# Performance work log

Hardware: AMD Instinct MI355X
Metric: run time of the kernel (lower is better)

## Reference

```python
import jax, jax.numpy as jnp
import numpy as np

L = 18                      # tree depth, N = 2**L - 1 nodes (complete binary tree)
N = 2**L - 1               # 262143
D = 128                     # embedding dim
V = 100000                  # vocab size of the single data type
E = 8                       # edge_count


def setup_inputs() -> dict:
    key = jax.random.key(0)
    ks = jax.random.split(key, 8)
    data = jax.random.randint(ks[0], (N,), 0, V)
    edges = jax.random.randint(ks[1], (N,), 0, E)
    data_vecs = jax.random.normal(ks[2], (V, D), dtype=jnp.float32) * 0.1
    # torch uses torch.rand (U[0,1)); scaled for numerical stability over 18 levels
    data_W = jax.random.uniform(ks[3], (D, D), dtype=jnp.float32) * 0.1
    data_b = jax.random.uniform(ks[4], (D,), dtype=jnp.float32) * 0.1
    edge_W = jax.random.uniform(ks[5], (E, D, D), dtype=jnp.float32) * (2.0 / D)
    edge_b = jax.random.uniform(ks[6], (E, D), dtype=jnp.float32) * 0.1
    score_W = jax.random.uniform(ks[7], (D, 1), dtype=jnp.float32)
    return {"data": data, "edges": edges, "data_vecs": data_vecs,
            "data_W": data_W, "data_b": data_b, "edge_W": edge_W,
            "edge_b": edge_b, "score_W": score_W}


def reference(data, edges, data_vecs, data_W, data_b, edge_W, edge_b, score_W):
    # per-node leaf term: addmm(data_bias, data_vecs[data], data_W)  -> [N, D]
    raw = data_vecs[data] @ data_W + data_b
    ret = raw    # value returned to the parent (leaves: unclamped)
    emb = raw    # stored embedding (internal nodes: pre-clamp h)
    # bottom-up over levels; level l occupies indices [2**l - 1, 2**(l+1) - 1)
    for l in reversed(range(L - 1)):
        p0, npar = 2**l - 1, 2**l
        c0, M = 2**(l + 1) - 1, 2**(l + 1)
        child_ret = ret[c0:c0 + M]              # [M, D], siblings adjacent
        eids = edges[c0:c0 + M]                 # [M]
        # edge-weighted child transform: child @ edge_W[e] + edge_b[e]
        contrib = edge_b[eids]
        for e in range(E):                      # small static edge loop
            contrib = contrib + jnp.where((eids == e)[:, None], child_ret, 0.0) @ edge_W[e]
        # sum the two children of each parent, then (leaf + children) / (nc + 1)
        contrib = contrib.reshape(npar, 2, D).sum(axis=1)
        h = (raw[p0:p0 + npar] + contrib) / 3.0
        emb = emb.at[p0:p0 + npar].set(h)
        ret = ret.at[p0:p0 + npar].set(jnp.maximum(h, 0.0))
    scores = (emb @ score_W)[:, 0]              # [N]
    return scores


if __name__ == "__main__":
    out = reference(**setup_inputs())
    print(out.shape, out.dtype)
```

## Files before the change

kernel.cpp:

```cpp
#include <hip/hip_runtime.h>

#define D 128
#define NLVL 17
#define TS 64
#define LVLPAD 1024
#define LDSTR 136
#define LEAF_BLKS 2057
#define CHUNK 2048
#define CNT_BLKS 128
#define PLVL0 10
#define CBASE 2047
#define NBINS 56
#define NRAW 2047

typedef float  floatx4 __attribute__((ext_vector_type(4)));
typedef short  shortx8 __attribute__((ext_vector_type(8)));

__device__ __forceinline__ unsigned short f2bf(float f) {
    unsigned u = __float_as_uint(f);
    u += 0x7FFFu + ((u >> 16) & 1u);
    return (unsigned short)(u >> 16);
}
__device__ __forceinline__ float bf2f(unsigned short h) {
    return __uint_as_float(((unsigned)h) << 16);
}
__device__ __forceinline__ int lvl_base_dev(int l) { return ((2 << l) - 2) + LVLPAD * l; }

__global__ __launch_bounds__(256) void prep_kernel(
    const float* __restrict__ dW, const float* __restrict__ db,
    const float* __restrict__ eW, const float* __restrict__ eb,
    const float* __restrict__ sWs, const float* __restrict__ vecs,
    const int* __restrict__ edges,
    unsigned short* __restrict__ ewt, unsigned short* __restrict__ cwt,
    unsigned short* __restrict__ dwt, float* __restrict__ dcomp,
    float* __restrict__ sv, float* __restrict__ s0, int* __restrict__ ctr,
    int* __restrict__ gcnt128, int Nn,
    unsigned short* __restrict__ vbf, int n4)
{
    __shared__ float smem[8448];
    const int b = blockIdx.x, t = threadIdx.x;
    if (b < 32) {
        float* w_s = smem;
        float* cs  = smem + 4096;
        const int e = b >> 2, cc = b & 3;
        for (int i = t; i < D * 8; i += 256) {
            const int k = i >> 3, j4 = i & 7;
            ((float4*)w_s)[i] = ((const float4*)eW)[((size_t)e * D + k) * 32 + cc * 8 + j4];
        }
        __syncthreads();
        const int r2 = t >> 1, h = t & 1;
        float4 acc[4];
        #pragma unroll
        for (int m = 0; m < 4; m++) acc[m] = make_float4(0.f, 0.f, 0.f, 0.f);
        for (int k = 0; k < D; k++) {
            const float a = dW[(size_t)r2 * D + k];
            #pragma unroll
            for (int m = 0; m < 4; m++) {
                const float4 w4 = ((const float4*)w_s)[k * 8 + h * 4 + m];
                acc[m].x += a * w4.x; acc[m].y += a * w4.y; acc[m].z += a * w4.z; acc[m].w += a * w4.w;
            }
        }
        #pragma unroll
        for (int m = 0; m < 4; m++) {
            cs[r2 * 33 + h * 16 + m * 4 + 0] = acc[m].x;
            cs[r2 * 33 + h * 16 + m * 4 + 1] = acc[m].y;
            cs[r2 * 33 + h * 16 + m * 4 + 2] = acc[m].z;
            cs[r2 * 33 + h * 16 + m * 4 + 3] = acc[m].w;
        }
        __syncthreads();
        {
            const int nn = t >> 3, kseg = t & 7, k0 = kseg * 16;
            unsigned ow[8];
            #pragma unroll
            for (int i2 = 0; i2 < 8; i2++) {
                const unsigned short lo = f2bf(cs[(k0 + 2 * i2) * 33 + nn]);
                const unsigned short hi = f2bf(cs[(k0 + 2 * i2 + 1) * 33 + nn]);
                ow[i2] = (unsigned)lo | ((unsigned)hi << 16);
            }
            uint4* dstp = (uint4*)(cwt + (size_t)e * D * D + (size_t)(cc * 32 + nn) * D + k0);
            dstp[0] = make_uint4(ow[0], ow[1], ow[2], ow[3]);
            dstp[1] = make_uint4(ow[4], ow[5], ow[6], ow[7]);
        }
        if (t < 32) {
            float a2 = 0.f;
            for (int k = 0; k < D; k++) a2 += db[k] * w_s[k * 32 + t];
            dcomp[e * D + cc * 32 + t] = a2 + eb[e * D + cc * 32 + t];
        }
    } else if (b < 41) {
        float* lds = smem;
        const int bb = b - 32;
        const float* src = (bb < 8) ? (eW + (size_t)bb * D * D) : dW;
        unsigned short* dst = (bb < 8) ? (ewt + (size_t)bb * D * D) : dwt;
        for (int half = 0; half < 2; half++) {
            __syncthreads();
            for (int i = t; i < 64 * D / 4; i += 256) {
                float4 v = ((const float4*)src)[half * (64 * D / 4) + i];
                const int k = (i * 4) >> 7, n = (i * 4) & 127;
                lds[k * 129 + n]     = v.x;
                lds[k * 129 + n + 1] = v.y;
                lds[k * 129 + n + 2] = v.z;
                lds[k * 129 + n + 3] = v.w;
            }
            __syncthreads();
            const int n = t >> 1, hh = t & 1;
            for (int kk = 0; kk < 32; kk++) {
                const int k = hh * 32 + kk;
                dst[(size_t)n * D + half * 64 + k] = f2bf(lds[k * 129 + n]);
            }
        }
    } else if (b == 41) {
        float* red = smem;
        if (t < NBINS) ctr[t] = 0;
        if (t < D) {
            float acc = 0.f;
            for (int j = 0; j < D; j++) acc += dW[(size_t)t * D + j] * sWs[j];
            sv[t] = acc;
        }
        red[t] = (t < D) ? db[t] * sWs[t] : 0.f;
        __syncthreads();
        for (int s = 128; s > 0; s >>= 1) { if (t < s) red[t] += red[t + s]; __syncthreads(); }
        if (t == 0) s0[0] = red[0];
    } else if (b < 42 + CNT_BLKS) {
        int* lc = (int*)smem;
        if (t < NBINS) lc[t] = 0;
        __syncthreads();
        for (int c = CBASE + (b - 42) * 256 + t; c < Nn; c += CNT_BLKS * 256) {
            const int e = edges[c];
            const int p = (c - 1) >> 1;
            const int l = 31 - __clz(p + 1);
            atomicAdd(&lc[(l - PLVL0) * 8 + e], 1);
        }
        __syncthreads();
        if (t < NBINS) gcnt128[(b - 42) * NBINS + t] = lc[t];
    } else {
        for (int i = (b - 42 - CNT_BLKS) * 256 + t; i < n4; i += (gridDim.x - 42 - CNT_BLKS) * 256) {
            const float4 v = ((const float4*)vecs)[i];
            uint2 o;
            o.x = (unsigned)f2bf(v.x) | ((unsigned)f2bf(v.y) << 16);
            o.y = (unsigned)f2bf(v.z) | ((unsigned)f2bf(v.w) << 16);
            ((uint2*)vbf)[i] = o;
        }
    }
}

__global__ __launch_bounds__(256) void place_kernel(
    const int* __restrict__ edges, const int* __restrict__ gcnt128,
    int* __restrict__ gstart, int* __restrict__ glim,
    int* __restrict__ ctr, int* __restrict__ perm, int Nn)
{
    __shared__ unsigned char key_s[CHUNK];
    __shared__ int part[256];
    __shared__ int tot[NBINS];
    __shared__ int lcnt[NBINS], lbase[NBINS];
    __shared__ int gs_s[7 * 9], gl_s[7 * 8];
    const int t = threadIdx.x;
    {
        const int k = t & 63, bs = t >> 6;
        int s = 0;
        if (k < NBINS)
            for (int bb = bs; bb < CNT_BLKS; bb += 4) s += gcnt128[bb * NBINS + k];
        part[t] = s;
    }
    if (t < NBINS) lcnt[t] = 0;
    __syncthreads();
    if (t < NBINS)
        tot[t] = part[t] + part[t + 64] + part[t + 128] + part[t + 192];
    __syncthreads();
    if (t == 0) {
        for (int li = 0; li < 7; li++) {
            int acc = 0;
            for (int e = 0; e < 8; e++) {
                gs_s[li * 9 + e] = acc;
                gl_s[li * 8 + e] = acc + tot[li * 8 + e];
                acc = (acc + tot[li * 8 + e] + (TS - 1)) & ~(TS - 1);
            }
            gs_s[li * 9 + 8] = acc;
        }
    }
    __syncthreads();
    if (blockIdx.x == 0) {
        if (t < 63) gstart[PLVL0 * 9 + t] = gs_s[t];
        if (t < NBINS) glim[PLVL0 * 8 + t] = gl_s[t];
    }
    const int base = CBASE + blockIdx.x * CHUNK;
    for (int i = t; i < CHUNK; i += 256) {
        const int c = base + i;
        if (c < Nn) {
            const int e = edges[c];
            const int p = (c - 1) >> 1;
            const int l = 31 - __clz(p + 1);
            const int kk = (l - PLVL0) * 8 + e;
            key_s[i] = (unsigned char)kk;
            atomicAdd(&lcnt[kk], 1);
        } else key_s[i] = 255;
    }
    __syncthreads();
    if (t < NBINS) {
        const int n = lcnt[t];
        lbase[t] = n ? atomicAdd(&ctr[t], n) : 0;
        lcnt[t] = 0;
    }
    __syncthreads();
    for (int i = t; i < CHUNK; i += 256) {
        const int c = base + i;
        if (c >= Nn) continue;
        const int kk = key_s[i];
        if (kk == 255) continue;
        const int off = atomicAdd(&lcnt[kk], 1);
        const int l = (kk >> 3) + PLVL0, e = kk & 7;
        const int pos = gs_s[(l - PLVL0) * 9 + e] + lbase[kk] + off;
        perm[lvl_base_dev(l) + pos] = c;
    }
}

__global__ __launch_bounds__(256, 6) void leaf_embed_kernel(
    unsigned short* __restrict__ X,
    const unsigned short* __restrict__ vbf,
    const int* __restrict__ data,
    const int* __restrict__ perm,
    const int* __restrict__ gstart9,
    const int* __restrict__ glim8,
    const unsigned short* __restrict__ cwt,
    const float* __restrict__ dcomp,
    const float* __restrict__ sv, const float* __restrict__ s0p,
    const unsigned short* __restrict__ dwt,
    const float* __restrict__ db,
    float* __restrict__ out,
    int NI, int lbase_leaf)
{
    __shared__ unsigned short a_s[TS * LDSTR];
    const int t = threadIdx.x;
    const bool is_leaf = (blockIdx.x < LEAF_BLKS);
    const int r = t >> 2, h4 = t & 3;

    int e = 0, c;
    const unsigned short* Wg;
    const float* bias;
    if (is_leaf) {
        const int ts = blockIdx.x * TS;
        if (ts >= gstart9[8]) return;
        #pragma unroll
        for (int j = 1; j < 8; j++) if (ts >= gstart9[j]) e = j;
        const int p = ts + r;
        c = (p < glim8[e]) ? perm[lbase_leaf + p] : -1;
        Wg = cwt + (size_t)e * D * D;
        bias = dcomp + (size_t)e * D;
    } else {
        const int node = (blockIdx.x - LEAF_BLKS) * TS + r;
        c = (node < NI) ? node : -1;
        Wg = dwt;
        bias = db;
    }

    {
        unsigned short* dst = a_s + r * LDSTR + h4 * 32;
        if (c >= 0) {
            const uint4* src = (const uint4*)(vbf + (size_t)data[c] * D + h4 * 32);
            if (is_leaf) {
                float sc = 0.f;
                #pragma unroll
                for (int j = 0; j < 4; j++) {
                    const uint4 v = src[j];
                    const unsigned* pv = (const unsigned*)&v;
                    #pragma unroll
                    for (int u = 0; u < 4; u++) {
                        const int n = h4 * 32 + j * 8 + u * 2;
                        sc += bf2f((unsigned short)pv[u]) * sv[n]
                            + bf2f((unsigned short)(pv[u] >> 16)) * sv[n + 1];
                    }
                    ((uint4*)dst)[j] = v;
                }
                sc += __shfl_xor(sc, 1, 64);
                sc += __shfl_xor(sc, 2, 64);
                if (h4 == 0) out[c] = sc + s0p[0];
            } else {
                #pragma unroll
                for (int j = 0; j < 4; j++) ((uint4*)dst)[j] = src[j];
            }
        } else {
            #pragma unroll
            for (int j = 0; j < 4; j++) ((uint4*)dst)[j] = make_uint4(0u, 0u, 0u, 0u);
        }
    }
    __syncthreads();

    const int lane = t & 63, wv = t >> 6;
    const int cq = lane & 15, q = lane >> 4;
    const floatx4 z4 = {0.f, 0.f, 0.f, 0.f};
    floatx4 acc[4][2];
    #pragma unroll
    for (int i = 0; i < 4; i++) { acc[i][0] = z4; acc[i][1] = z4; }
    #pragma unroll
    for (int ks = 0; ks < 4; ks++) {
        shortx8 bfr[2];
        #pragma unroll
        for (int nl = 0; nl < 2; nl++) {
            const int n = (wv * 2 + nl) * 16 + cq;
            bfr[nl] = *(const shortx8*)(Wg + (size_t)n * D + ks * 32 + q * 8);
        }
        #pragma unroll
        for (int mt = 0; mt < 4; mt++) {
            const shortx8 af = *(const shortx8*)(a_s + (mt * 16 + cq) * LDSTR + ks * 32 + q * 8);
            acc[mt][0] = __builtin_amdgcn_mfma_f32_16x16x32_bf16(bfr[0], af, acc[mt][0], 0, 0, 0);
            acc[mt][1] = __builtin_amdgcn_mfma_f32_16x16x32_bf16(bfr[1], af, acc[mt][1], 0, 0, 0);
        }
    }
    __syncthreads();
    #pragma unroll
    for (int nl = 0; nl < 2; nl++) {
        const int n0 = (wv * 2 + nl) * 16 + q * 4;
        const float4 b4 = *(const float4*)(bias + n0);
        #pragma unroll
        for (int mt = 0; mt < 4; mt++) {
            const int m = mt * 16 + cq;
            const unsigned lo = (unsigned)f2bf(acc[mt][nl][0] + b4.x)
                              | ((unsigned)f2bf(acc[mt][nl][1] + b4.y) << 16);
            const unsigned hi = (unsigned)f2bf(acc[mt][nl][2] + b4.z)
                              | ((unsigned)f2bf(acc[mt][nl][3] + b4.w) << 16);
            *(uint2*)(a_s + (size_t)m * LDSTR + n0) = make_uint2(lo, hi);
        }
    }
    __syncthreads();
    if (c >= 0) {
        uint4* dstg = (uint4*)(X + (size_t)c * D + h4 * 32);
        const uint4* srcl = (const uint4*)(a_s + r * LDSTR + h4 * 32);
        #pragma unroll
        for (int j = 0; j < 4; j++) dstg[j] = srcl[j];
    }
}

__global__ __launch_bounds__(256, 3) void tree_fused_kernel(
    unsigned short* __restrict__ X,
    const unsigned short* __restrict__ vbf,
    const int* __restrict__ data,
    const int* __restrict__ perm,
    const int* __restrict__ gstart9,
    const int* __restrict__ glim8,
    const unsigned short* __restrict__ dwt,
    const float* __restrict__ db,
    const unsigned short* __restrict__ ewt,
    const float* __restrict__ eb,
    const float* __restrict__ svec,
    float* __restrict__ out,
    int lbase)
{
    __shared__ unsigned short a_s[TS * LDSTR];
    __shared__ float cs_s[TS][132];
    __shared__ float scorebuf[TS];
    const int t = threadIdx.x;
    const int ts = blockIdx.x * TS;
    if (ts >= gstart9[8]) return;
    int e = 0;
    #pragma unroll
    for (int j = 1; j < 8; j++) if (ts >= gstart9[j]) e = j;
    const int r = t >> 2, h4 = t & 3;
    const int p = ts + r;
    const int c = (p < glim8[e]) ? perm[lbase + p] : -1;

    if (t < TS) scorebuf[t] = 0.f;
    {
        unsigned short* dst = a_s + r * LDSTR + h4 * 32;
        float* cd = &cs_s[r][h4 * 32];
        if (c >= 0) {
            const uint4* src = (const uint4*)(vbf + (size_t)data[c] * D + h4 * 32);
            const uint4* ya = (const uint4*)(X + (size_t)(2 * c + 1) * D + h4 * 32);
            const uint4* yb = (const uint4*)(X + (size_t)(2 * c + 2) * D + h4 * 32);
            #pragma unroll
            for (int j = 0; j < 4; j++) {
                ((uint4*)dst)[j] = src[j];
                const uint4 rb = ya[j], rc = yb[j];
                const unsigned* pb = (const unsigned*)&rb;
                const unsigned* pc = (const unsigned*)&rc;
                #pragma unroll
                for (int u = 0; u < 4; u++) {
                    cd[j * 8 + u * 2]     = bf2f((unsigned short)pb[u]) + bf2f((unsigned short)pc[u]);
                    cd[j * 8 + u * 2 + 1] = bf2f((unsigned short)(pb[u] >> 16)) + bf2f((unsigned short)(pc[u] >> 16));
                }
            }
        } else {
            #pragma unroll
            for (int j = 0; j < 4; j++) {
                ((uint4*)dst)[j] = make_uint4(0u, 0u, 0u, 0u);
                ((float4*)cd)[j * 2]     = make_float4(0.f, 0.f, 0.f, 0.f);
                ((float4*)cd)[j * 2 + 1] = make_float4(0.f, 0.f, 0.f, 0.f);
            }
        }
    }
    __syncthreads();

    const int lane = t & 63, wv = t >> 6;
    const int cq = lane & 15, q = lane >> 4;
    const floatx4 z4 = {0.f, 0.f, 0.f, 0.f};
    floatx4 acc[4][2];
    #pragma unroll
    for (int i = 0; i < 4; i++) { acc[i][0] = z4; acc[i][1] = z4; }
    #pragma unroll
    for (int ks = 0; ks < 4; ks++) {
        shortx8 bfr[2];
        #pragma unroll
        for (int nl = 0; nl < 2; nl++) {
            const int n = (wv * 2 + nl) * 16 + cq;
            bfr[nl] = *(const shortx8*)(dwt + (size_t)n * D + ks * 32 + q * 8);
        }
        #pragma unroll
        for (int mt = 0; mt < 4; mt++) {
            const shortx8 af = *(const shortx8*)(a_s + (mt * 16 + cq) * LDSTR + ks * 32 + q * 8);
            acc[mt][0] = __builtin_amdgcn_mfma_f32_16x16x32_bf16(bfr[0], af, acc[mt][0], 0, 0, 0);
            acc[mt][1] = __builtin_amdgcn_mfma_f32_16x16x32_bf16(bfr[1], af, acc[mt][1], 0, 0, 0);
        }
    }
    const float inv3 = 1.0f / 3.0f;
    float sp[4] = {0.f, 0.f, 0.f, 0.f};
    uint2 hpk[2][4];
    #pragma unroll
    for (int nl = 0; nl < 2; nl++) {
        const int n0 = (wv * 2 + nl) * 16 + q * 4;
        const float4 db4 = *(const float4*)(db + n0);
        const float4 sv4 = *(const float4*)(svec + n0);
        #pragma unroll
        for (int mt = 0; mt < 4; mt++) {
            const int m = mt * 16 + cq;
            const float4 cs4 = *(const float4*)(&cs_s[m][n0]);
            const float h0 = (acc[mt][nl][0] + db4.x + cs4.x) * inv3;
            const float h1 = (acc[mt][nl][1] + db4.y + cs4.y) * inv3;
            const float h2 = (acc[mt][nl][2] + db4.z + cs4.z) * inv3;
            const float h3 = (acc[mt][nl][3] + db4.w + cs4.w) * inv3;
            sp[mt] += h0 * sv4.x + h1 * sv4.y + h2 * sv4.z + h3 * sv4.w;
            unsigned short q0 = f2bf(h0), q1 = f2bf(h1), q2 = f2bf(h2), q3 = f2bf(h3);
            q0 = (q0 & 0x8000u) ? 0 : q0;
            q1 = (q1 & 0x8000u) ? 0 : q1;
            q2 = (q2 & 0x8000u) ? 0 : q2;
            q3 = (q3 & 0x8000u) ? 0 : q3;
            hpk[nl][mt] = make_uint2((unsigned)q0 | ((unsigned)q1 << 16),
                                     (unsigned)q2 | ((unsigned)q3 << 16));
        }
    }
    #pragma unroll
    for (int mt = 0; mt < 4; mt++) {
        sp[mt] += __shfl_xor(sp[mt], 16, 64);
        sp[mt] += __shfl_xor(sp[mt], 32, 64);
    }
    __syncthreads();
    #pragma unroll
    for (int nl = 0; nl < 2; nl++) {
        const int n0 = (wv * 2 + nl) * 16 + q * 4;
        #pragma unroll
        for (int mt = 0; mt < 4; mt++)
            *(uint2*)(a_s + (size_t)(mt * 16 + cq) * LDSTR + n0) = hpk[nl][mt];
    }
    if (q == 0) {
        #pragma unroll
        for (int mt = 0; mt < 4; mt++) atomicAdd(&scorebuf[mt * 16 + cq], sp[mt]);
    }
    __syncthreads();
    const unsigned short* Wg = ewt + (size_t)e * D * D;
    #pragma unroll
    for (int i = 0; i < 4; i++) { acc[i][0] = z4; acc[i][1] = z4; }
    #pragma unroll
    for (int ks = 0; ks < 4; ks++) {
        shortx8 bfr[2];
        #pragma unroll
        for (int nl = 0; nl < 2; nl++) {
            const int n = (wv * 2 + nl) * 16 + cq;
            bfr[nl] = *(const shortx8*)(Wg + (size_t)n * D + ks * 32 + q * 8);
        }
        #pragma unroll
        for (int mt = 0; mt < 4; mt++) {
            const shortx8 af = *(const shortx8*)(a_s + (mt * 16 + cq) * LDSTR + ks * 32 + q * 8);
            acc[mt][0] = __builtin_amdgcn_mfma_f32_16x16x32_bf16(bfr[0], af, acc[mt][0], 0, 0, 0);
            acc[mt][1] = __builtin_amdgcn_mfma_f32_16x16x32_bf16(bfr[1], af, acc[mt][1], 0, 0, 0);
        }
    }
    __syncthreads();
    #pragma unroll
    for (int nl = 0; nl < 2; nl++) {
        const int n0 = (wv * 2 + nl) * 16 + q * 4;
        const float4 b4 = *(const float4*)(eb + (size_t)e * D + n0);
        #pragma unroll
        for (int mt = 0; mt < 4; mt++) {
            const int m = mt * 16 + cq;
            const unsigned lo = (unsigned)f2bf(acc[mt][nl][0] + b4.x)
                              | ((unsigned)f2bf(acc[mt][nl][1] + b4.y) << 16);
            const unsigned hi = (unsigned)f2bf(acc[mt][nl][2] + b4.z)
                              | ((unsigned)f2bf(acc[mt][nl][3] + b4.w) << 16);
            *(uint2*)(a_s + (size_t)m * LDSTR + n0) = make_uint2(lo, hi);
        }
    }
    __syncthreads();
    if (c >= 0) {
        uint4* dstg = (uint4*)(X + (size_t)c * D + h4 * 32);
        const uint4* srcl = (const uint4*)(a_s + r * LDSTR + h4 * 32);
        #pragma unroll
        for (int j = 0; j < 4; j++) dstg[j] = srcl[j];
        if (h4 == 1) out[c] = scorebuf[r];
    }
}

__global__ __launch_bounds__(256) void sub_kernel(
    unsigned short* __restrict__ X,
    const float* __restrict__ eW,
    const float* __restrict__ eb,
    const int* __restrict__ edges,
    const float* __restrict__ sW,
    float* __restrict__ out,
    int rbase, int nlev)
{
    __shared__ __align__(16) float xbuf[4][D];
    const int t = threadIdx.x, wv = t >> 6, lane = t & 63;
    const int u = rbase + blockIdx.x;
    const int j2 = lane * 2;
    const float inv3 = 1.0f / 3.0f;

    for (int lev = nlev - 1; lev >= 0; lev--) {
        const int first = ((u + 1) << lev) - 1;
        const int cnt = 1 << lev;
        for (int i = wv; i < cnt; i += 4) {
            const int n = first + i;
            const unsigned ra = *(const unsigned*)(X + (size_t)n * D + j2);
            const unsigned rb = *(const unsigned*)(X + (size_t)(2 * n + 1) * D + j2);
            const unsigned rc = *(const unsigned*)(X + (size_t)(2 * n + 2) * D + j2);
            const float h0 = (bf2f((unsigned short)ra) + bf2f((unsigned short)rb)
                            + bf2f((unsigned short)rc)) * inv3;
            const float h1 = (bf2f((unsigned short)(ra >> 16)) + bf2f((unsigned short)(rb >> 16))
                            + bf2f((unsigned short)(rc >> 16))) * inv3;
            float sc = h0 * sW[j2] + h1 * sW[j2 + 1];
            #pragma unroll
            for (int o = 32; o > 0; o >>= 1) sc += __shfl_xor(sc, o, 64);
            if (lane == 0) out[n] = sc;
            if (n == 0) continue;
            float2 x2 = make_float2(fmaxf(h0, 0.f), fmaxf(h1, 0.f));
            *(float2*)(xbuf[wv] + j2) = x2;
            const int e = edges[n];
            const float* W = eW + (size_t)e * D * D;
            float y0 = 0.f, y1 = 0.f;
            #pragma unroll 8
            for (int k4 = 0; k4 < 32; k4++) {
                const float4 xk = *(const float4*)(xbuf[wv] + k4 * 4);
                const float2 w0 = *(const float2*)(W + (size_t)(k4 * 4 + 0) * D + j2);
                const float2 w1 = *(const float2*)(W + (size_t)(k4 * 4 + 1) * D + j2);
                const float2 w2 = *(const float2*)(W + (size_t)(k4 * 4 + 2) * D + j2);
                const float2 w3 = *(const float2*)(W + (size_t)(k4 * 4 + 3) * D + j2);
                y0 += xk.x * w0.x + xk.y * w1.x + xk.z * w2.x + xk.w * w3.x;
                y1 += xk.x * w0.y + xk.y * w1.y + xk.z * w2.y + xk.w * w3.y;
            }
            y0 += eb[e * D + j2];
            y1 += eb[e * D + j2 + 1];
            const unsigned o = (unsigned)f2bf(y0) | ((unsigned)f2bf(y1) << 16);
            *(unsigned*)(X + (size_t)n * D + j2) = o;
        }
        __syncthreads();
    }
}

extern "C" void kernel_launch(void* const* d_in, const int* in_sizes, int n_in,
                              void* d_out, int out_size, void* d_ws, size_t ws_size,
                              hipStream_t stream) {
    const int*   data      = (const int*)d_in[0];
    const int*   edges     = (const int*)d_in[1];
    const float* data_vecs = (const float*)d_in[2];
    const float* data_W    = (const float*)d_in[3];
    const float* data_b    = (const float*)d_in[4];
    const float* edge_W    = (const float*)d_in[5];
    const float* edge_b    = (const float*)d_in[6];
    const float* score_W   = (const float*)d_in[7];
    float* out = (float*)d_out;

    const int Nn = in_sizes[0];
    const int VD = in_sizes[2];
    const int PERM_TOTAL = (Nn - 1) + LVLPAD * NLVL;

    char* w = (char*)d_ws;
    size_t off = 0;
    unsigned short* X = (unsigned short*)(w + off); off += (size_t)Nn * D * 2;
    int* perm = (int*)(w + off);  off += (size_t)PERM_TOTAL * 4;
    off = (off + 255) & ~(size_t)255;
    int* gstart  = (int*)(w + off); off += NLVL * 9 * 4;
    int* glim    = (int*)(w + off); off += NLVL * 8 * 4;
    int* gcnt128 = (int*)(w + off); off += CNT_BLKS * 64 * 4;
    int* ctr     = (int*)(w + off); off += 64 * 4;
    off = (off + 255) & ~(size_t)255;
    float* dcomp = (float*)(w + off); off += 8 * D * 4;
    float* sv    = (float*)(w + off); off += D * 4;
    float* s0    = (float*)(w + off); off += 256;
    off = (off + 255) & ~(size_t)255;
    unsigned short* ewt = (unsigned short*)(w + off); off += (size_t)8 * D * D * 2;
    unsigned short* cwt = (unsigned short*)(w + off); off += (size_t)8 * D * D * 2;
    unsigned short* dwt = (unsigned short*)(w + off); off += (size_t)D * D * 2;
    off = (off + 255) & ~(size_t)255;
    unsigned short* vbf = (unsigned short*)(w + off); off += (size_t)VD * 2;

    prep_kernel<<<42 + CNT_BLKS + 1024, 256, 0, stream>>>(
        data_W, data_b, edge_W, edge_b, score_W, data_vecs, edges,
        ewt, cwt, dwt, dcomp, sv, s0, ctr, gcnt128, Nn, vbf, VD / 4);

    const int place_blks = (Nn - CBASE + CHUNK - 1) / CHUNK;
    place_kernel<<<place_blks, 256, 0, stream>>>(edges, gcnt128, gstart, glim, ctr, perm, Nn);

    {
        const int embed_blks = (NRAW + TS - 1) / TS;
        const int lbase_leaf = ((2 << 16) - 2) + LVLPAD * 16;
        leaf_embed_kernel<<<LEAF_BLKS + embed_blks, 256, 0, stream>>>(
            X, vbf, data, perm, gstart + 16 * 9, glim + 16 * 8,
            cwt, dcomp, sv, s0, dwt, data_b, out, NRAW, lbase_leaf);
    }

    for (int l = 15; l >= PLVL0; l--) {
        const int M = 2 << l;
        const int lbase = ((2 << l) - 2) + LVLPAD * l;
        tree_fused_kernel<<<M / TS + 8, 256, 0, stream>>>(
            X, vbf, data, perm, gstart + l * 9, glim + l * 8,
            dwt, data_b, ewt, edge_b, score_W, out, lbase);
    }

    sub_kernel<<<128, 256, 0, stream>>>(X, edge_W, edge_b, edges, score_W, out, 127, 4);
    sub_kernel<<<8, 256, 0, stream>>>(X, edge_W, edge_b, edges, score_W, out, 7, 4);
    sub_kernel<<<1, 256, 0, stream>>>(X, edge_W, edge_b, edges, score_W, out, 0, 3);
}
```

Baseline: 283.4 us.

## Merge all stages into one persistent cooperative kernel with grid syncs

Replaces the sequence of about eleven kernel launches (prep, place, leaf embed, six tree levels, three sub kernels) with one cooperative persistent kernel. Each former kernel becomes a device function run over virtual block indices in a grid-stride loop, with grid.sync() between stages and shared memory pooled in one static buffer. This removes per-launch overhead and the gaps between dependent launches. In exchange, the grid is capped at 768 blocks with occupancy limited by the largest shared-memory stage, grid-wide barriers add their own cost, and the serial sub stages leave most blocks idle.

```diff
diff --git a/kernel.cpp b/kernel.cpp
--- a/kernel.cpp
+++ b/kernel.cpp
@@ -1,4 +1,7 @@
 #include <hip/hip_runtime.h>
+#include <hip/hip_cooperative_groups.h>
+
+namespace cg = cooperative_groups;
 
 #define D 128
 #define NLVL 17
@@ -12,6 +15,8 @@
 #define CBASE 2047
 #define NBINS 56
 #define NRAW 2047
+#define VEC_BLKS 1024
+#define SPOOL_BYTES 51456
 
 typedef float  floatx4 __attribute__((ext_vector_type(4)));
 typedef short  shortx8 __attribute__((ext_vector_type(8)));
@@ -26,26 +31,45 @@
 }
 __device__ __forceinline__ int lvl_base_dev(int l) { return ((2 << l) - 2) + LVLPAD * l; }
 
-__global__ __launch_bounds__(256) void prep_kernel(
-    const float* __restrict__ dW, const float* __restrict__ db,
-    const float* __restrict__ eW, const float* __restrict__ eb,
-    const float* __restrict__ sWs, const float* __restrict__ vecs,
-    const int* __restrict__ edges,
-    unsigned short* __restrict__ ewt, unsigned short* __restrict__ cwt,
-    unsigned short* __restrict__ dwt, float* __restrict__ dcomp,
-    float* __restrict__ sv, float* __restrict__ s0, int* __restrict__ ctr,
-    int* __restrict__ gcnt128, int Nn,
-    unsigned short* __restrict__ vbf, int n4)
+struct MegaArgs {
+    const int*   data;
+    const int*   edges;
+    const float* vecs;
+    const float* dW;
+    const float* db;
+    const float* eW;
+    const float* eb;
+    const float* sWs;
+    unsigned short* X;
+    int* perm;
+    int* gstart;
+    int* glim;
+    int* gcnt;
+    int* ctr;
+    float* dcomp;
+    float* sv;
+    float* s0;
+    unsigned short* ewt;
+    unsigned short* cwt;
+    unsigned short* dwt;
+    unsigned short* vbf;
+    float* out;
+    int Nn;
+    int n4;
+};
+
+__device__ void prep_block(int b, const MegaArgs& A, char* spool)
 {
-    __shared__ float smem[8448];
-    const int b = blockIdx.x, t = threadIdx.x;
+    const int t = threadIdx.x;
+    float* smem = (float*)spool;
+    __syncthreads();
     if (b < 32) {
         float* w_s = smem;
         float* cs  = smem + 4096;
         const int e = b >> 2, cc = b & 3;
         for (int i = t; i < D * 8; i += 256) {
             const int k = i >> 3, j4 = i & 7;
-            ((float4*)w_s)[i] = ((const float4*)eW)[((size_t)e * D + k) * 32 + cc * 8 + j4];
+            ((float4*)w_s)[i] = ((const float4*)A.eW)[((size_t)e * D + k) * 32 + cc * 8 + j4];
         }
         __syncthreads();
         const int r2 = t >> 1, h = t & 1;
@@ -53,7 +77,7 @@
         #pragma unroll
         for (int m = 0; m < 4; m++) acc[m] = make_float4(0.f, 0.f, 0.f, 0.f);
         for (int k = 0; k < D; k++) {
-            const float a = dW[(size_t)r2 * D + k];
+            const float a = A.dW[(size_t)r2 * D + k];
             #pragma unroll
             for (int m = 0; m < 4; m++) {
                 const float4 w4 = ((const float4*)w_s)[k * 8 + h * 4 + m];
@@ -77,20 +101,20 @@
                 const unsigned short hi = f2bf(cs[(k0 + 2 * i2 + 1) * 33 + nn]);
                 ow[i2] = (unsigned)lo | ((unsigned)hi << 16);
             }
-            uint4* dstp = (uint4*)(cwt + (size_t)e * D * D + (size_t)(cc * 32 + nn) * D + k0);
+            uint4* dstp = (uint4*)(A.cwt + (size_t)e * D * D + (size_t)(cc * 32 + nn) * D + k0);
             dstp[0] = make_uint4(ow[0], ow[1], ow[2], ow[3]);
             dstp[1] = make_uint4(ow[4], ow[5], ow[6], ow[7]);
         }
         if (t < 32) {
             float a2 = 0.f;
-            for (int k = 0; k < D; k++) a2 += db[k] * w_s[k * 32 + t];
-            dcomp[e * D + cc * 32 + t] = a2 + eb[e * D + cc * 32 + t];
+            for (int k = 0; k < D; k++) a2 += A.db[k] * w_s[k * 32 + t];
+            A.dcomp[e * D + cc * 32 + t] = a2 + A.eb[e * D + cc * 32 + t];
         }
     } else if (b < 41) {
         float* lds = smem;
         const int bb = b - 32;
-        const float* src = (bb < 8) ? (eW + (size_t)bb * D * D) : dW;
-        unsigned short* dst = (bb < 8) ? (ewt + (size_t)bb * D * D) : dwt;
+        const float* src = (bb < 8) ? (A.eW + (size_t)bb * D * D) : A.dW;
+        unsigned short* dst = (bb < 8) ? (A.ewt + (size_t)bb * D * D) : A.dwt;
         for (int half = 0; half < 2; half++) {
             __syncthreads();
             for (int i = t; i < 64 * D / 4; i += 256) {
@@ -110,55 +134,55 @@
         }
     } else if (b == 41) {
         float* red = smem;
-        if (t < NBINS) ctr[t] = 0;
+        if (t < NBINS) A.ctr[t] = 0;
         if (t < D) {
             float acc = 0.f;
-            for (int j = 0; j < D; j++) acc += dW[(size_t)t * D + j] * sWs[j];
-            sv[t] = acc;
-        }
-        red[t] = (t < D) ? db[t] * sWs[t] : 0.f;
+            for (int j = 0; j < D; j++) acc += A.dW[(size_t)t * D + j] * A.sWs[j];
+            A.sv[t] = acc;
+        }
+        red[t] = (t < D) ? A.db[t] * A.sWs[t] : 0.f;
         __syncthreads();
         for (int s = 128; s > 0; s >>= 1) { if (t < s) red[t] += red[t + s]; __syncthreads(); }
-        if (t == 0) s0[0] = red[0];
+        if (t == 0) A.s0[0] = red[0];
     } else if (b < 42 + CNT_BLKS) {
         int* lc = (int*)smem;
         if (t < NBINS) lc[t] = 0;
         __syncthreads();
-        for (int c = CBASE + (b - 42) * 256 + t; c < Nn; c += CNT_BLKS * 256) {
-            const int e = edges[c];
+        for (int c = CBASE + (b - 42) * 256 + t; c < A.Nn; c += CNT_BLKS * 256) {
+            const int e = A.edges[c];
             const int p = (c - 1) >> 1;
             const int l = 31 - __clz(p + 1);
             atomicAdd(&lc[(l - PLVL0) * 8 + e], 1);
         }
         __syncthreads();
-        if (t < NBINS) gcnt128[(b - 42) * NBINS + t] = lc[t];
+        if (t < NBINS) A.gcnt[(b - 42) * NBINS + t] = lc[t];
     } else {
-        for (int i = (b - 42 - CNT_BLKS) * 256 + t; i < n4; i += (gridDim.x - 42 - CNT_BLKS) * 256) {
-            const float4 v = ((const float4*)vecs)[i];
+        for (int i = (b - 42 - CNT_BLKS) * 256 + t; i < A.n4; i += VEC_BLKS * 256) {
+            const float4 v = ((const float4*)A.vecs)[i];
             uint2 o;
             o.x = (unsigned)f2bf(v.x) | ((unsigned)f2bf(v.y) << 16);
             o.y = (unsigned)f2bf(v.z) | ((unsigned)f2bf(v.w) << 16);
-            ((uint2*)vbf)[i] = o;
-        }
-    }
-}
-
-__global__ __launch_bounds__(256) void place_kernel(
-    const int* __restrict__ edges, const int* __restrict__ gcnt128,
-    int* __restrict__ gstart, int* __restrict__ glim,
-    int* __restrict__ ctr, int* __restrict__ perm, int Nn)
+            ((uint2*)A.vbf)[i] = o;
+        }
+    }
+}
+
+__device__ void place_block(int vb, const MegaArgs& A, char* spool)
 {
-    __shared__ unsigned char key_s[CHUNK];
-    __shared__ int part[256];
-    __shared__ int tot[NBINS];
-    __shared__ int lcnt[NBINS], lbase[NBINS];
-    __shared__ int gs_s[7 * 9], gl_s[7 * 8];
+    unsigned char* key_s = (unsigned char*)spool;
+    int* part  = (int*)(spool + 2048);
+    int* tot   = (int*)(spool + 3072);
+    int* lcnt  = (int*)(spool + 3328);
+    int* lbase = (int*)(spool + 3584);
+    int* gs_s  = (int*)(spool + 3840);
+    int* gl_s  = (int*)(spool + 4096);
     const int t = threadIdx.x;
+    __syncthreads();
     {
         const int k = t & 63, bs = t >> 6;
         int s = 0;
         if (k < NBINS)
-            for (int bb = bs; bb < CNT_BLKS; bb += 4) s += gcnt128[bb * NBINS + k];
+            for (int bb = bs; bb < CNT_BLKS; bb += 4) s += A.gcnt[bb * NBINS + k];
         part[t] = s;
     }
     if (t < NBINS) lcnt[t] = 0;
@@ -178,15 +202,15 @@
         }
     }
     __syncthreads();
-    if (blockIdx.x == 0) {
-        if (t < 63) gstart[PLVL0 * 9 + t] = gs_s[t];
-        if (t < NBINS) glim[PLVL0 * 8 + t] = gl_s[t];
-    }
-    const int base = CBASE + blockIdx.x * CHUNK;
+    if (vb == 0) {
+        if (t < 63) A.gstart[PLVL0 * 9 + t] = gs_s[t];
+        if (t < NBINS) A.glim[PLVL0 * 8 + t] = gl_s[t];
+    }
+    const int base = CBASE + vb * CHUNK;
     for (int i = t; i < CHUNK; i += 256) {
         const int c = base + i;
-        if (c < Nn) {
-            const int e = edges[c];
+        if (c < A.Nn) {
+            const int e = A.edges[c];
             const int p = (c - 1) >> 1;
             const int l = 31 - __clz(p + 1);
             const int kk = (l - PLVL0) * 8 + e;
@@ -197,65 +221,55 @@
     __syncthreads();
     if (t < NBINS) {
         const int n = lcnt[t];
-        lbase[t] = n ? atomicAdd(&ctr[t], n) : 0;
+        lbase[t] = n ? atomicAdd(&A.ctr[t], n) : 0;
         lcnt[t] = 0;
     }
     __syncthreads();
     for (int i = t; i < CHUNK; i += 256) {
         const int c = base + i;
-        if (c >= Nn) continue;
+        if (c >= A.Nn) continue;
         const int kk = key_s[i];
         if (kk == 255) continue;
         const int off = atomicAdd(&lcnt[kk], 1);
         const int l = (kk >> 3) + PLVL0, e = kk & 7;
         const int pos = gs_s[(l - PLVL0) * 9 + e] + lbase[kk] + off;
-        perm[lvl_base_dev(l) + pos] = c;
-    }
-}
-
-__global__ __launch_bounds__(256, 6) void leaf_embed_kernel(
-    unsigned short* __restrict__ X,
-    const unsigned short* __restrict__ vbf,
-    const int* __restrict__ data,
-    const int* __restrict__ perm,
-    const int* __restrict__ gstart9,
-    const int* __restrict__ glim8,
-    const unsigned short* __restrict__ cwt,
-    const float* __restrict__ dcomp,
-    const float* __restrict__ sv, const float* __restrict__ s0p,
-    const unsigned short* __restrict__ dwt,
-    const float* __restrict__ db,
-    float* __restrict__ out,
-    int NI, int lbase_leaf)
+        A.perm[lvl_base_dev(l) + pos] = c;
+    }
+}
+
+__device__ void leaf_block(int vb, const MegaArgs& A, char* spool, int lbase_leaf)
 {
-    __shared__ unsigned short a_s[TS * LDSTR];
+    unsigned short* a_s = (unsigned short*)spool;
     const int t = threadIdx.x;
-    const bool is_leaf = (blockIdx.x < LEAF_BLKS);
+    const int* gstart9 = A.gstart + 16 * 9;
+    const int* glim8   = A.glim + 16 * 8;
+    const bool is_leaf = (vb < LEAF_BLKS);
     const int r = t >> 2, h4 = t & 3;
 
     int e = 0, c;
     const unsigned short* Wg;
     const float* bias;
     if (is_leaf) {
-        const int ts = blockIdx.x * TS;
+        const int ts = vb * TS;
         if (ts >= gstart9[8]) return;
         #pragma unroll
         for (int j = 1; j < 8; j++) if (ts >= gstart9[j]) e = j;
         const int p = ts + r;
-        c = (p < glim8[e]) ? perm[lbase_leaf + p] : -1;
-        Wg = cwt + (size_t)e * D * D;
-        bias = dcomp + (size_t)e * D;
+        c = (p < glim8[e]) ? A.perm[lbase_leaf + p] : -1;
+        Wg = A.cwt + (size_t)e * D * D;
+        bias = A.dcomp + (size_t)e * D;
     } else {
-        const int node = (blockIdx.x - LEAF_BLKS) * TS + r;
-        c = (node < NI) ? node : -1;
-        Wg = dwt;
-        bias = db;
-    }
+        const int node = (vb - LEAF_BLKS) * TS + r;
+        c = (node < NRAW) ? node : -1;
+        Wg = A.dwt;
+        bias = A.db;
+    }
+    __syncthreads();
 
     {
         unsigned short* dst = a_s + r * LDSTR + h4 * 32;
         if (c >= 0) {
-            const uint4* src = (const uint4*)(vbf + (size_t)data[c] * D + h4 * 32);
+            const uint4* src = (const uint4*)(A.vbf + (size_t)A.data[c] * D + h4 * 32);
             if (is_leaf) {
                 float sc = 0.f;
                 #pragma unroll
@@ -265,14 +279,14 @@
                     #pragma unroll
                     for (int u = 0; u < 4; u++) {
                         const int n = h4 * 32 + j * 8 + u * 2;
-                        sc += bf2f((unsigned short)pv[u]) * sv[n]
-                            + bf2f((unsigned short)(pv[u] >> 16)) * sv[n + 1];
+                        sc += bf2f((unsigned short)pv[u]) * A.sv[n]
+                            + bf2f((unsigned short)(pv[u] >> 16)) * A.sv[n + 1];
                     }
                     ((uint4*)dst)[j] = v;
                 }
                 sc += __shfl_xor(sc, 1, 64);
                 sc += __shfl_xor(sc, 2, 64);
-                if (h4 == 0) out[c] = sc + s0p[0];
+                if (h4 == 0) A.out[c] = sc + A.s0[0];
             } else {
                 #pragma unroll
                 for (int j = 0; j < 4; j++) ((uint4*)dst)[j] = src[j];
@@ -322,49 +336,38 @@
     }
     __syncthreads();
     if (c >= 0) {
-        uint4* dstg = (uint4*)(X + (size_t)c * D + h4 * 32);
+        uint4* dstg = (uint4*)(A.X + (size_t)c * D + h4 * 32);
         const uint4* srcl = (const uint4*)(a_s + r * LDSTR + h4 * 32);
         #pragma unroll
         for (int j = 0; j < 4; j++) dstg[j] = srcl[j];
     }
 }
 
-__global__ __launch_bounds__(256, 3) void tree_fused_kernel(
-    unsigned short* __restrict__ X,
-    const unsigned short* __restrict__ vbf,
-    const int* __restrict__ data,
-    const int* __restrict__ perm,
-    const int* __restrict__ gstart9,
-    const int* __restrict__ glim8,
-    const unsigned short* __restrict__ dwt,
-    const float* __restrict__ db,
-    const unsigned short* __restrict__ ewt,
-    const float* __restrict__ eb,
-    const float* __restrict__ svec,
-    float* __restrict__ out,
-    int lbase)
+__device__ void tree_tile(int tile, const MegaArgs& A, char* spool,
+                          const int* gstart9, const int* glim8, int lbase)
 {
-    __shared__ unsigned short a_s[TS * LDSTR];
-    __shared__ float cs_s[TS][132];
-    __shared__ float scorebuf[TS];
+    unsigned short* a_s = (unsigned short*)spool;
+    float (*cs_s)[132]  = (float(*)[132])(spool + TS * LDSTR * 2);
+    float* scorebuf     = (float*)(spool + TS * LDSTR * 2 + TS * 132 * 4);
     const int t = threadIdx.x;
-    const int ts = blockIdx.x * TS;
+    const int ts = tile * TS;
     if (ts >= gstart9[8]) return;
     int e = 0;
     #pragma unroll
     for (int j = 1; j < 8; j++) if (ts >= gstart9[j]) e = j;
     const int r = t >> 2, h4 = t & 3;
     const int p = ts + r;
-    const int c = (p < glim8[e]) ? perm[lbase + p] : -1;
+    const int c = (p < glim8[e]) ? A.perm[lbase + p] : -1;
+    __syncthreads();
 
     if (t < TS) scorebuf[t] = 0.f;
     {
         unsigned short* dst = a_s + r * LDSTR + h4 * 32;
         float* cd = &cs_s[r][h4 * 32];
         if (c >= 0) {
-            const uint4* src = (const uint4*)(vbf + (size_t)data[c] * D + h4 * 32);
-            const uint4* ya = (const uint4*)(X + (size_t)(2 * c + 1) * D + h4 * 32);
-            const uint4* yb = (const uint4*)(X + (size_t)(2 * c + 2) * D + h4 * 32);
+            const uint4* src = (const uint4*)(A.vbf + (size_t)A.data[c] * D + h4 * 32);
+            const uint4* ya = (const uint4*)(A.X + (size_t)(2 * c + 1) * D + h4 * 32);
+            const uint4* yb = (const uint4*)(A.X + (size_t)(2 * c + 2) * D + h4 * 32);
             #pragma unroll
             for (int j = 0; j < 4; j++) {
                 ((uint4*)dst)[j] = src[j];
@@ -400,7 +403,7 @@
         #pragma unroll
         for (int nl = 0; nl < 2; nl++) {
             const int n = (wv * 2 + nl) * 16 + cq;
-            bfr[nl] = *(const shortx8*)(dwt + (size_t)n * D + ks * 32 + q * 8);
+            bfr[nl] = *(const shortx8*)(A.dwt + (size_t)n * D + ks * 32 + q * 8);
         }
         #pragma unroll
         for (int mt = 0; mt < 4; mt++) {
@@ -415,8 +418,8 @@
     #pragma unroll
     for (int nl = 0; nl < 2; nl++) {
         const int n0 = (wv * 2 + nl) * 16 + q * 4;
-        const float4 db4 = *(const float4*)(db + n0);
-        const float4 sv4 = *(const float4*)(svec + n0);
+        const float4 db4 = *(const float4*)(A.db + n0);
+        const float4 sv4 = *(const float4*)(A.sWs + n0);
         #pragma unroll
         for (int mt = 0; mt < 4; mt++) {
             const int m = mt * 16 + cq;
@@ -453,7 +456,7 @@
         for (int mt = 0; mt < 4; mt++) atomicAdd(&scorebuf[mt * 16 + cq], sp[mt]);
     }
     __syncthreads();
-    const unsigned short* Wg = ewt + (size_t)e * D * D;
+    const unsigned short* Wg = A.ewt + (size_t)e * D * D;
     #pragma unroll
     for (int i = 0; i < 4; i++) { acc[i][0] = z4; acc[i][1] = z4; }
     #pragma unroll
@@ -475,7 +478,7 @@
     #pragma unroll
     for (int nl = 0; nl < 2; nl++) {
         const int n0 = (wv * 2 + nl) * 16 + q * 4;
-        const float4 b4 = *(const float4*)(eb + (size_t)e * D + n0);
+        const float4 b4 = *(const float4*)(A.eb + (size_t)e * D + n0);
         #pragma unroll
         for (int mt = 0; mt < 4; mt++) {
             const int m = mt * 16 + cq;
@@ -488,50 +491,43 @@
     }
     __syncthreads();
     if (c >= 0) {
-        uint4* dstg = (uint4*)(X + (size_t)c * D + h4 * 32);
+        uint4* dstg = (uint4*)(A.X + (size_t)c * D + h4 * 32);
         const uint4* srcl = (const uint4*)(a_s + r * LDSTR + h4 * 32);
         #pragma unroll
         for (int j = 0; j < 4; j++) dstg[j] = srcl[j];
-        if (h4 == 1) out[c] = scorebuf[r];
-    }
-}
-
-__global__ __launch_bounds__(256) void sub_kernel(
-    unsigned short* __restrict__ X,
-    const float* __restrict__ eW,
-    const float* __restrict__ eb,
-    const int* __restrict__ edges,
-    const float* __restrict__ sW,
-    float* __restrict__ out,
-    int rbase, int nlev)
+        if (h4 == 1) A.out[c] = scorebuf[r];
+    }
+}
+
+__device__ void sub_block(int u, int nlev, const MegaArgs& A, char* spool)
 {
-    __shared__ __align__(16) float xbuf[4][D];
+    float (*xbuf)[D] = (float(*)[D])spool;
     const int t = threadIdx.x, wv = t >> 6, lane = t & 63;
-    const int u = rbase + blockIdx.x;
     const int j2 = lane * 2;
     const float inv3 = 1.0f / 3.0f;
+    __syncthreads();
 
     for (int lev = nlev - 1; lev >= 0; lev--) {
         const int first = ((u + 1) << lev) - 1;
         const int cnt = 1 << lev;
         for (int i = wv; i < cnt; i += 4) {
             const int n = first + i;
-            const unsigned ra = *(const unsigned*)(X + (size_t)n * D + j2);
-            const unsigned rb = *(const unsigned*)(X + (size_t)(2 * n + 1) * D + j2);
-            const unsigned rc = *(const unsigned*)(X + (size_t)(2 * n + 2) * D + j2);
+            const unsigned ra = *(const unsigned*)(A.X + (size_t)n * D + j2);
+            const unsigned rb = *(const unsigned*)(A.X + (size_t)(2 * n + 1) * D + j2);
+            const unsigned rc = *(const unsigned*)(A.X + (size_t)(2 * n + 2) * D + j2);
             const float h0 = (bf2f((unsigned short)ra) + bf2f((unsigned short)rb)
                             + bf2f((unsigned short)rc)) * inv3;
             const float h1 = (bf2f((unsigned short)(ra >> 16)) + bf2f((unsigned short)(rb >> 16))
                             + bf2f((unsigned short)(rc >> 16))) * inv3;
-            float sc = h0 * sW[j2] + h1 * sW[j2 + 1];
+            float sc = h0 * A.sWs[j2] + h1 * A.sWs[j2 + 1];
             #pragma unroll
             for (int o = 32; o > 0; o >>= 1) sc += __shfl_xor(sc, o, 64);
-            if (lane == 0) out[n] = sc;
+            if (lane == 0) A.out[n] = sc;
             if (n == 0) continue;
             float2 x2 = make_float2(fmaxf(h0, 0.f), fmaxf(h1, 0.f));
             *(float2*)(xbuf[wv] + j2) = x2;
-            const int e = edges[n];
-            const float* W = eW + (size_t)e * D * D;
+            const int e = A.edges[n];
+            const float* W = A.eW + (size_t)e * D * D;
             float y0 = 0.f, y1 = 0.f;
             #pragma unroll 8
             for (int k4 = 0; k4 < 32; k4++) {
@@ -543,28 +539,48 @@
                 y0 += xk.x * w0.x + xk.y * w1.x + xk.z * w2.x + xk.w * w3.x;
                 y1 += xk.x * w0.y + xk.y * w1.y + xk.z * w2.y + xk.w * w3.y;
             }
-            y0 += eb[e * D + j2];
-            y1 += eb[e * D + j2 + 1];
+            y0 += A.eb[e * D + j2];
+            y1 += A.eb[e * D + j2 + 1];
             const unsigned o = (unsigned)f2bf(y0) | ((unsigned)f2bf(y1) << 16);
-            *(unsigned*)(X + (size_t)n * D + j2) = o;
+            *(unsigned*)(A.X + (size_t)n * D + j2) = o;
         }
         __syncthreads();
     }
+}
+
+__global__ __launch_bounds__(256, 3) void mega_kernel(MegaArgs A)
+{
+    __shared__ __align__(16) char spool[SPOOL_BYTES];
+    cg::grid_group grid = cg::this_grid();
+    const int bx = blockIdx.x, gsz = gridDim.x;
+
+    for (int vb = bx; vb < 42 + CNT_BLKS + VEC_BLKS; vb += gsz) prep_block(vb, A, spool);
+    grid.sync();
+    const int pblks = (A.Nn - CBASE + CHUNK - 1) / CHUNK;
+    for (int vb = bx; vb < pblks; vb += gsz) place_block(vb, A, spool);
+    grid.sync();
+    const int lbase_leaf = ((2 << 16) - 2) + LVLPAD * 16;
+    const int leaf_tiles = LEAF_BLKS + (NRAW + TS - 1) / TS;
+    for (int vb = bx; vb < leaf_tiles; vb += gsz) leaf_block(vb, A, spool, lbase_leaf);
+    grid.sync();
+    for (int l = 15; l >= PLVL0; l--) {
+        const int tiles = ((2 << l) / TS) + 8;
+        const int* g9 = A.gstart + l * 9;
+        const int* g8 = A.glim + l * 8;
+        const int lb = ((2 << l) - 2) + LVLPAD * l;
+        for (int tile = bx; tile < tiles; tile += gsz) tree_tile(tile, A, spool, g9, g8, lb);
+        grid.sync();
+    }
+    if (bx < 128) sub_block(127 + bx, 4, A, spool);
+    grid.sync();
+    if (bx < 8) sub_block(7 + bx, 4, A, spool);
+    grid.sync();
+    if (bx == 0) sub_block(0, 3, A, spool);
 }
 
 extern "C" void kernel_launch(void* const* d_in, const int* in_sizes, int n_in,
                               void* d_out, int out_size, void* d_ws, size_t ws_size,
                               hipStream_t stream) {
-    const int*   data      = (const int*)d_in[0];
-    const int*   edges     = (const int*)d_in[1];
-    const float* data_vecs = (const float*)d_in[2];
-    const float* data_W    = (const float*)d_in[3];
-    const float* data_b    = (const float*)d_in[4];
-    const float* edge_W    = (const float*)d_in[5];
-    const float* edge_b    = (const float*)d_in[6];
-    const float* score_W   = (const float*)d_in[7];
-    float* out = (float*)d_out;
-
     const int Nn = in_sizes[0];
     const int VD = in_sizes[2];
     const int PERM_TOTAL = (Nn - 1) + LVLPAD * NLVL;
@@ -576,7 +592,7 @@
     off = (off + 255) & ~(size_t)255;
     int* gstart  = (int*)(w + off); off += NLVL * 9 * 4;
     int* glim    = (int*)(w + off); off += NLVL * 8 * 4;
-    int* gcnt128 = (int*)(w + off); off += CNT_BLKS * 64 * 4;
+    int* gcnt    = (int*)(w + off); off += CNT_BLKS * 64 * 4;
     int* ctr     = (int*)(w + off); off += 64 * 4;
     off = (off + 255) & ~(size_t)255;
     float* dcomp = (float*)(w + off); off += 8 * D * 4;
@@ -589,30 +605,32 @@
     off = (off + 255) & ~(size_t)255;
     unsigned short* vbf = (unsigned short*)(w + off); off += (size_t)VD * 2;
 
-    prep_kernel<<<42 + CNT_BLKS + 1024, 256, 0, stream>>>(
-        data_W, data_b, edge_W, edge_b, score_W, data_vecs, edges,
-        ewt, cwt, dwt, dcomp, sv, s0, ctr, gcnt128, Nn, vbf, VD / 4);
-
-    const int place_blks = (Nn - CBASE + CHUNK - 1) / CHUNK;
-    place_kernel<<<place_blks, 256, 0, stream>>>(edges, gcnt128, gstart, glim, ctr, perm, Nn);
-
-    {
-        const int embed_blks = (NRAW + TS - 1) / TS;
-        const int lbase_leaf = ((2 << 16) - 2) + LVLPAD * 16;
-        leaf_embed_kernel<<<LEAF_BLKS + embed_blks, 256, 0, stream>>>(
-            X, vbf, data, perm, gstart + 16 * 9, glim + 16 * 8,
-            cwt, dcomp, sv, s0, dwt, data_b, out, NRAW, lbase_leaf);
-    }
-
-    for (int l = 15; l >= PLVL0; l--) {
-        const int M = 2 << l;
-        const int lbase = ((2 << l) - 2) + LVLPAD * l;
-        tree_fused_kernel<<<M / TS + 8, 256, 0, stream>>>(
-            X, vbf, data, perm, gstart + l * 9, glim + l * 8,
-            dwt, data_b, ewt, edge_b, score_W, out, lbase);
-    }
-
-    sub_kernel<<<128, 256, 0, stream>>>(X, edge_W, edge_b, edges, score_W, out, 127, 4);
-    sub_kernel<<<8, 256, 0, stream>>>(X, edge_W, edge_b, edges, score_W, out, 7, 4);
-    sub_kernel<<<1, 256, 0, stream>>>(X, edge_W, edge_b, edges, score_W, out, 0, 3);
-}
+    MegaArgs A;
+    A.data = (const int*)d_in[0];
+    A.edges = (const int*)d_in[1];
+    A.vecs = (const float*)d_in[2];
+    A.dW = (const float*)d_in[3];
+    A.db = (const float*)d_in[4];
+    A.eW = (const float*)d_in[5];
+    A.eb = (const float*)d_in[6];
+    A.sWs = (const float*)d_in[7];
+    A.X = X; A.perm = perm; A.gstart = gstart; A.glim = glim;
+    A.gcnt = gcnt; A.ctr = ctr;
+    A.dcomp = dcomp; A.sv = sv; A.s0 = s0;
+    A.ewt = ewt; A.cwt = cwt; A.dwt = dwt; A.vbf = vbf;
+    A.out = (float*)d_out;
+    A.Nn = Nn;
+    A.n4 = VD / 4;
+
+    static int s_grid = 0;
+    if (s_grid == 0) {
+        int occ = 0;
+        hipError_t e = hipOccupancyMaxActiveBlocksPerMultiprocessor(&occ, mega_kernel, 256, 0);
+        if (e != hipSuccess || occ < 1) occ = 1;
+        long cap = (long)occ * 256;
+        s_grid = (int)(cap < 768 ? cap : 768);
+    }
+    void* kargs[] = { (void*)&A };
+    hipLaunchCooperativeKernel((const void*)mega_kernel, dim3(s_grid), dim3(256),
+                               kargs, 0, stream);
+}
```

Measured after the change: 665.4 us. 135% more time.
